# Kernel tuning notes

Measured on AMD Instinct MI355X. Metric: run time of the kernel, lower is better.

Reference implementation:

```python
import jax, jax.numpy as jnp
import numpy as np

B, NQ, NK = 8, 1024, 1024
DQ = DK = DV = 512
H = 8
DH = DV // H
EPS = 1e-5
NEG = -1e9


def _layer_norm(x, g, b):
    mu = jnp.mean(x, axis=-1, keepdims=True)
    var = jnp.mean(jnp.square(x - mu), axis=-1, keepdims=True)
    return (x - mu) * jax.lax.rsqrt(var + EPS) * g + b


def setup_inputs() -> dict:
    key = jax.random.key(0)
    ks = jax.random.split(key, 16)
    s_q = 1.0 / np.sqrt(DQ)
    s_k = 1.0 / np.sqrt(DK)
    s_v = 1.0 / np.sqrt(DV)
    return {
        "Q": jax.random.normal(ks[0], (B, NQ, DQ), jnp.float32),
        "K": jax.random.normal(ks[1], (B, NK, DK), jnp.float32),
        "mask": jax.random.randint(ks[2], (B, NK), 0, 2, jnp.int32),
        "Wq": jax.random.uniform(ks[3], (DQ, DV), jnp.float32, -s_q, s_q),
        "bq": jax.random.uniform(ks[4], (DV,), jnp.float32, -s_q, s_q),
        "Wk": jax.random.uniform(ks[5], (DK, DV), jnp.float32, -s_k, s_k),
        "bk": jax.random.uniform(ks[6], (DV,), jnp.float32, -s_k, s_k),
        "Wv": jax.random.uniform(ks[7], (DK, DV), jnp.float32, -s_k, s_k),
        "bv": jax.random.uniform(ks[8], (DV,), jnp.float32, -s_k, s_k),
        "Wo": jax.random.uniform(ks[9], (DV, DV), jnp.float32, -s_v, s_v),
        "bo": jax.random.uniform(ks[10], (DV,), jnp.float32, -s_v, s_v),
        "g0": jnp.ones((DV,), jnp.float32),
        "b0": jnp.zeros((DV,), jnp.float32),
        "g1": jnp.ones((DV,), jnp.float32),
        "b1": jnp.zeros((DV,), jnp.float32),
    }


def reference(Q, K, mask, Wq, bq, Wk, bk, Wv, bv, Wo, bo, g0, b0, g1, b1):
    b = Q.shape[0]
    # projections: [B, N, DV] -> [B, N, H, DH]
    q = (Q @ Wq + bq).reshape(b, -1, H, DH)
    k = (K @ Wk + bk).reshape(b, -1, H, DH)
    v = (K @ Wv + bv).reshape(b, -1, H, DH)
    scores = jnp.einsum("bqhd,bkhd->bhqk", q, k) / np.sqrt(DH)  # [B,H,Nq,Nk]
    scores = jnp.where((mask == 0)[:, None, None, :], NEG, scores)
    A = jax.nn.softmax(scores, axis=-1)
    o = q + jnp.einsum("bhqk,bkhd->bqhd", A, v)  # residual on projected Q (per head)
    O = o.reshape(b, -1, DV)
    O = _layer_norm(O, g0, b0)
    O = O + jax.nn.relu(O @ Wo + bo)
    O = _layer_norm(O, g1, b1)
    return O
```

## Files before the change

kernel.cpp:

```cpp
#include <hip/hip_runtime.h>


typedef float f32x4 __attribute__((ext_vector_type(4)));
typedef short bf16x8 __attribute__((ext_vector_type(8)));
typedef unsigned short u16;

#define MFMA16 __builtin_amdgcn_mfma_f32_16x16x32_bf16

__device__ __forceinline__ float bf2f(u16 u){
    unsigned x = ((unsigned)u) << 16;
    return __builtin_bit_cast(float, x);
}
__device__ __forceinline__ u16 f2bf(float f){
    unsigned u = __builtin_bit_cast(unsigned, f);
    u = u + 0x7fffu + ((u >> 16) & 1u);
    return (u16)(u >> 16);
}

__global__ __launch_bounds__(256) void transpose_w(
    const float* __restrict__ Wq, const float* __restrict__ Wk,
    const float* __restrict__ Wv, const float* __restrict__ Wo,
    u16* __restrict__ wt)
{
    const int z = blockIdx.z;
    const float* W = (z == 0) ? Wq : (z == 1) ? Wk : (z == 2) ? Wv : Wo;
    u16* out = wt + (size_t)z * 512 * 512;

    __shared__ u16 tile[32][33];
    const int k0 = blockIdx.y * 32, n0 = blockIdx.x * 32;
    const int c = threadIdx.x & 31, r = threadIdx.x >> 5;
#pragma unroll
    for (int i = 0; i < 4; i++) {
        int rr = r + i * 8;
        tile[rr][c] = f2bf(W[(size_t)(k0 + rr) * 512 + n0 + c]);
    }
    __syncthreads();
#pragma unroll
    for (int i = 0; i < 4; i++) {
        int rr = r + i * 8;
        out[(size_t)(n0 + rr) * 512 + k0 + c] = tile[c][rr];
    }
}

__global__ __launch_bounds__(256) void transpose_v(
    const u16* __restrict__ vb, u16* __restrict__ vtg)
{
    __shared__ u16 tile[32][33];
    const int bh = blockIdx.z;
    const int b = bh >> 3, h = bh & 7;
    const int k0 = blockIdx.x * 32, d0 = blockIdx.y * 32;
    const int c = threadIdx.x & 31, r = threadIdx.x >> 5;
#pragma unroll
    for (int i = 0; i < 4; i++) {
        int rr = r + i * 8;
        tile[rr][c] = vb[(size_t)(b * 1024 + k0 + rr) * 512 + h * 64 + d0 + c];
    }
    __syncthreads();
#pragma unroll
    for (int i = 0; i < 4; i++) {
        int rr = r + i * 8;
        vtg[(size_t)(bh * 64 + d0 + rr) * 1024 + k0 + c] = tile[c][rr];
    }
}

__global__ __launch_bounds__(256) void gemm_proj(
    const float* __restrict__ Q, const float* __restrict__ K,
    const u16* __restrict__ wt,
    const float* __restrict__ bq, const float* __restrict__ bk, const float* __restrict__ bv,
    u16* __restrict__ qb, u16* __restrict__ kb, u16* __restrict__ vb)
{
    __shared__ __align__(16) u16 lds_a[128 * 40];
    __shared__ __align__(16) u16 lds_b[128 * 40];

    const int z = blockIdx.z;
    const float* X = (z == 0) ? Q : K;
    const u16* Wt = wt + (size_t)z * 512 * 512;
    const float* bias = (z == 0) ? bq : (z == 1) ? bk : bv;
    u16* outb = (z == 0) ? qb : (z == 1) ? kb : vb;

    const int bm = blockIdx.y, bn = blockIdx.x;
    const int t = threadIdx.x;
    const int wave = t >> 6, lane = t & 63, quad = lane >> 4, lm = lane & 15;
    const int wm = wave >> 1, wn = wave & 1;

    f32x4 acc[4][4];
    const f32x4 zz = {0.f, 0.f, 0.f, 0.f};
#pragma unroll
    for (int i = 0; i < 4; i++)
#pragma unroll
        for (int j = 0; j < 4; j++) acc[i][j] = zz;

    for (int k0 = 0; k0 < 512; k0 += 32) {
#pragma unroll
        for (int i = 0; i < 2; i++) {
            int idx = t + i * 256;
            int r = idx >> 2, c = (idx & 3) * 8;
            const float* xp = &X[(size_t)(bm * 128 + r) * 512 + k0 + c];
            f32x4 a0 = *(const f32x4*)xp;
            f32x4 a1 = *(const f32x4*)(xp + 4);
            bf16x8 xv;
#pragma unroll
            for (int j = 0; j < 4; j++) { xv[j] = (short)f2bf(a0[j]); xv[4 + j] = (short)f2bf(a1[j]); }
            *(bf16x8*)&lds_a[r * 40 + c] = xv;
            *(bf16x8*)&lds_b[r * 40 + c] =
                *(const bf16x8*)&Wt[(size_t)(bn * 128 + r) * 512 + k0 + c];
        }
        __syncthreads();
        bf16x8 af[4], bfr[4];
#pragma unroll
        for (int mi = 0; mi < 4; mi++)
            af[mi] = *(const bf16x8*)&lds_a[(wm * 64 + mi * 16 + lm) * 40 + quad * 8];
#pragma unroll
        for (int ni = 0; ni < 4; ni++)
            bfr[ni] = *(const bf16x8*)&lds_b[(wn * 64 + ni * 16 + lm) * 40 + quad * 8];
#pragma unroll
        for (int mi = 0; mi < 4; mi++)
#pragma unroll
            for (int ni = 0; ni < 4; ni++)
                acc[mi][ni] = MFMA16(af[mi], bfr[ni], acc[mi][ni], 0, 0, 0);
        __syncthreads();
    }

#pragma unroll
    for (int mi = 0; mi < 4; mi++) {
#pragma unroll
        for (int ni = 0; ni < 4; ni++) {
            const int col = bn * 128 + wn * 64 + ni * 16 + lm;
            const float bv_ = bias[col];
#pragma unroll
            for (int r = 0; r < 4; r++) {
                const int row = bm * 128 + wm * 64 + mi * 16 + quad * 4 + r;
                outb[(size_t)row * 512 + col] = f2bf(acc[mi][ni][r] + bv_);
            }
        }
    }
}

__global__ __launch_bounds__(256) void gemm_mlp(
    const u16* __restrict__ X, const u16* __restrict__ wt,
    const float* __restrict__ bo, const float* __restrict__ resid,
    float* __restrict__ outf)
{
    __shared__ __align__(16) u16 lds_a[128 * 40];
    __shared__ __align__(16) u16 lds_b[128 * 40];

    const u16* Wt = wt + (size_t)3 * 512 * 512;
    const int bm = blockIdx.y, bn = blockIdx.x;
    const int t = threadIdx.x;
    const int wave = t >> 6, lane = t & 63, quad = lane >> 4, lm = lane & 15;
    const int wm = wave >> 1, wn = wave & 1;

    f32x4 acc[4][4];
    const f32x4 zz = {0.f, 0.f, 0.f, 0.f};
#pragma unroll
    for (int i = 0; i < 4; i++)
#pragma unroll
        for (int j = 0; j < 4; j++) acc[i][j] = zz;

    for (int k0 = 0; k0 < 512; k0 += 32) {
#pragma unroll
        for (int i = 0; i < 2; i++) {
            int idx = t + i * 256;
            int r = idx >> 2, c = (idx & 3) * 8;
            *(bf16x8*)&lds_a[r * 40 + c] =
                *(const bf16x8*)&X[(size_t)(bm * 128 + r) * 512 + k0 + c];
            *(bf16x8*)&lds_b[r * 40 + c] =
                *(const bf16x8*)&Wt[(size_t)(bn * 128 + r) * 512 + k0 + c];
        }
        __syncthreads();
        bf16x8 af[4], bfr[4];
#pragma unroll
        for (int mi = 0; mi < 4; mi++)
            af[mi] = *(const bf16x8*)&lds_a[(wm * 64 + mi * 16 + lm) * 40 + quad * 8];
#pragma unroll
        for (int ni = 0; ni < 4; ni++)
            bfr[ni] = *(const bf16x8*)&lds_b[(wn * 64 + ni * 16 + lm) * 40 + quad * 8];
#pragma unroll
        for (int mi = 0; mi < 4; mi++)
#pragma unroll
            for (int ni = 0; ni < 4; ni++)
                acc[mi][ni] = MFMA16(af[mi], bfr[ni], acc[mi][ni], 0, 0, 0);
        __syncthreads();
    }

#pragma unroll
    for (int mi = 0; mi < 4; mi++) {
#pragma unroll
        for (int ni = 0; ni < 4; ni++) {
            const int col = bn * 128 + wn * 64 + ni * 16 + lm;
            const float bv_ = bo[col];
#pragma unroll
            for (int r = 0; r < 4; r++) {
                const int row = bm * 128 + wm * 64 + mi * 16 + quad * 4 + r;
                const size_t off = (size_t)row * 512 + col;
                outf[off] = resid[off] + fmaxf(acc[mi][ni][r] + bv_, 0.f);
            }
        }
    }
}

__global__ __launch_bounds__(256) void attn_kernel(
    const u16* __restrict__ qb, const u16* __restrict__ kb, const u16* __restrict__ vtg,
    const int* __restrict__ mask, float* __restrict__ O)
{
    __shared__ __align__(16) u16 k_tile[64 * 88];
    __shared__ __align__(16) u16 vt[64 * 88];
    __shared__ __align__(16) u16 p_st[4 * 32 * 88];
    __shared__ float mskf[1024];

    const int i = blockIdx.x;
    const int s_ = i >> 3;
    const int bh = (i & 7) + 8 * (s_ >> 3);
    const int qt = s_ & 7;
    const int b = bh >> 3, h = bh & 7;

    const int t = threadIdx.x, wave = t >> 6, lane = t & 63;
    const int quad = lane >> 4, lm = lane & 15;
    const int qbase = qt * 128 + wave * 32;
    const size_t baseb = (size_t)b * 1024 * 512;
    const size_t vbase = (size_t)((b * 8 + h) * 64) * 1024;

#pragma unroll
    for (int ii = 0; ii < 4; ii++) {
        int j = t + ii * 256;
        mskf[j] = mask[b * 1024 + j] ? 1.0f : 0.0f;
    }

    bf16x8 aq[2][2];
#pragma unroll
    for (int m = 0; m < 2; m++)
#pragma unroll
        for (int ks = 0; ks < 2; ks++)
            aq[m][ks] = *(const bf16x8*)&qb[baseb +
                (size_t)(qbase + m * 16 + lm) * 512 + h * 64 + ks * 32 + quad * 8];

    float lsum[2][4];
    f32x4 oacc[2][4];
    const f32x4 zz = {0.f, 0.f, 0.f, 0.f};
#pragma unroll
    for (int m = 0; m < 2; m++) {
#pragma unroll
        for (int r = 0; r < 4; r++) lsum[m][r] = 0.f;
#pragma unroll
        for (int c = 0; c < 4; c++) oacc[m][c] = zz;
    }

    const float SC2 = 0.125f * 1.44269504088896341f;
    const int srow = t >> 2, scol = (t & 3) * 16;
    u16* pw = &p_st[wave * 32 * 88];

    for (int kt = 0; kt < 16; ++kt) {
        const int keyg = kt * 64;
        {
            const u16* kp = &kb[baseb + (size_t)(keyg + srow) * 512 + h * 64 + scol];
            *(bf16x8*)&k_tile[srow * 88 + scol]     = *(const bf16x8*)kp;
            *(bf16x8*)&k_tile[srow * 88 + scol + 8] = *(const bf16x8*)(kp + 8);
            const u16* vp = &vtg[vbase + (size_t)srow * 1024 + keyg + scol];
            *(bf16x8*)&vt[srow * 88 + scol]     = *(const bf16x8*)vp;
            *(bf16x8*)&vt[srow * 88 + scol + 8] = *(const bf16x8*)(vp + 8);
        }
        __syncthreads();

        bf16x8 bk[4][2];
#pragma unroll
        for (int n = 0; n < 4; n++)
#pragma unroll
            for (int ks = 0; ks < 2; ks++)
                bk[n][ks] = *(const bf16x8*)&k_tile[(n * 16 + lm) * 88 + ks * 32 + quad * 8];

#pragma unroll
        for (int m = 0; m < 2; m++) {
#pragma unroll
            for (int n = 0; n < 4; n++) {
                f32x4 S = zz;
                S = MFMA16(aq[m][0], bk[n][0], S, 0, 0, 0);
                S = MFMA16(aq[m][1], bk[n][1], S, 0, 0, 0);
                const float mf = mskf[keyg + n * 16 + lm];
#pragma unroll
                for (int r = 0; r < 4; r++) {
                    float p = __builtin_amdgcn_exp2f(S[r] * SC2) * mf;
                    lsum[m][r] += p;
                    pw[(m * 16 + quad * 4 + r) * 88 + n * 16 + lm] = f2bf(p);
                }
            }
        }

#pragma unroll
        for (int m = 0; m < 2; m++) {
#pragma unroll
            for (int ks = 0; ks < 2; ks++) {
                bf16x8 ap = *(const bf16x8*)&pw[(m * 16 + lm) * 88 + ks * 32 + quad * 8];
#pragma unroll
                for (int c = 0; c < 4; c++) {
                    bf16x8 bv_ = *(const bf16x8*)&vt[(c * 16 + lm) * 88 + ks * 32 + quad * 8];
                    oacc[m][c] = MFMA16(ap, bv_, oacc[m][c], 0, 0, 0);
                }
            }
        }
        __syncthreads();
    }

#pragma unroll
    for (int m = 0; m < 2; m++)
#pragma unroll
        for (int r = 0; r < 4; r++) {
            float s = lsum[m][r];
            s += __shfl_xor(s, 1); s += __shfl_xor(s, 2);
            s += __shfl_xor(s, 4); s += __shfl_xor(s, 8);
            lsum[m][r] = s;
        }

#pragma unroll
    for (int m = 0; m < 2; m++)
#pragma unroll
        for (int c = 0; c < 4; c++)
#pragma unroll
            for (int r = 0; r < 4; r++) {
                const int row = qbase + m * 16 + quad * 4 + r;
                const int d = h * 64 + c * 16 + lm;
                const size_t off = baseb + (size_t)row * 512 + d;
                O[off] = bf2f(qb[off]) + oacc[m][c][r] / lsum[m][r];
            }
}

__global__ __launch_bounds__(256) void ln_kernel(
    const float* __restrict__ in, const float* __restrict__ g, const float* __restrict__ bsh,
    u16* __restrict__ outb, float* __restrict__ outf)
{
    const int row = blockIdx.x * 4 + (threadIdx.x >> 6);
    const int lane = threadIdx.x & 63;
    const float* x = in + (size_t)row * 512 + lane * 8;
    float v[8];
    *(f32x4*)&v[0] = *(const f32x4*)&x[0];
    *(f32x4*)&v[4] = *(const f32x4*)&x[4];
    float s = 0.f, sq = 0.f;
#pragma unroll
    for (int j = 0; j < 8; j++) { s += v[j]; sq += v[j] * v[j]; }
#pragma unroll
    for (int off = 1; off < 64; off <<= 1) {
        s += __shfl_xor(s, off);
        sq += __shfl_xor(sq, off);
    }
    const float mu = s * (1.f / 512.f);
    const float var = sq * (1.f / 512.f) - mu * mu;
    const float rs = rsqrtf(var + 1e-5f);
    float y[8];
#pragma unroll
    for (int j = 0; j < 8; j++) {
        int col = lane * 8 + j;
        y[j] = (v[j] - mu) * rs * g[col] + bsh[col];
    }
    if (outb != nullptr) {
        bf16x8 ov;
#pragma unroll
        for (int j = 0; j < 8; j++) ov[j] = (short)f2bf(y[j]);
        *(bf16x8*)&outb[(size_t)row * 512 + lane * 8] = ov;
    }
    if (outf != nullptr) {
        float* o = outf + (size_t)row * 512 + lane * 8;
        *(f32x4*)&o[0] = *(const f32x4*)&y[0];
        *(f32x4*)&o[4] = *(const f32x4*)&y[4];
    }
}

extern "C" void kernel_launch(void* const* d_in, const int* in_sizes, int n_in,
                              void* d_out, int out_size, void* d_ws, size_t ws_size,
                              hipStream_t stream) {
    const float* Q  = (const float*)d_in[0];
    const float* K  = (const float*)d_in[1];
    const int* mask = (const int*)d_in[2];
    const float* Wq = (const float*)d_in[3];
    const float* bq = (const float*)d_in[4];
    const float* Wk = (const float*)d_in[5];
    const float* bk = (const float*)d_in[6];
    const float* Wv = (const float*)d_in[7];
    const float* bv = (const float*)d_in[8];
    const float* Wo = (const float*)d_in[9];
    const float* bo = (const float*)d_in[10];
    const float* g0 = (const float*)d_in[11];
    const float* b0 = (const float*)d_in[12];
    const float* g1 = (const float*)d_in[13];
    const float* b1 = (const float*)d_in[14];
    float* out = (float*)d_out;

    char* ws = (char*)d_ws;
    const size_t MB = 1048576;
    u16*   wt  = (u16*)(ws);
    u16*   qb  = (u16*)(ws + 2 * MB);
    u16*   kb  = (u16*)(ws + 10 * MB);
    u16*   vtg = (u16*)(ws + 18 * MB);
    u16*   vb  = (u16*)(ws + 26 * MB);
    float* Of  = (float*)(ws + 26 * MB);
    u16*   O1b = (u16*)(ws + 2 * MB);
    float* O1f = (float*)(ws + 10 * MB);
    float* Uf  = (float*)(ws + 26 * MB);

    transpose_w<<<dim3(16, 16, 4), 256, 0, stream>>>(Wq, Wk, Wv, Wo, wt);
    gemm_proj<<<dim3(4, 64, 3), 256, 0, stream>>>(Q, K, wt, bq, bk, bv, qb, kb, vb);
    transpose_v<<<dim3(32, 2, 64), 256, 0, stream>>>(vb, vtg);
    attn_kernel<<<512, 256, 0, stream>>>(qb, kb, vtg, mask, Of);
    ln_kernel<<<2048, 256, 0, stream>>>(Of, g0, b0, O1b, O1f);
    gemm_mlp<<<dim3(4, 64, 1), 256, 0, stream>>>(O1b, wt, bo, O1f, Uf);
    ln_kernel<<<2048, 256, 0, stream>>>(Uf, g1, b1, nullptr, out);
}
```

Baseline: 207.1 us.

## Halve attention query tile, prefetch K/V tiles via registers, use additive mask bias

The attention kernel now gives each wave 16 query rows instead of 32 and doubles the grid to 1024 blocks, with launch bounds set to four blocks per CU. The next K/V tile is loaded into registers while the current one is computed, which hides global load latency behind compute. The multiplicative 0/1 mask becomes an additive -30000 bias folded into the exp2 FMA, and s_setprio raises wave priority around the MFMAs. In exchange, each K/V tile is reloaded by twice as many blocks, and the loop keeps four barriers per iteration pair.

```diff
diff --git a/kernel.cpp b/kernel.cpp
--- a/kernel.cpp
+++ b/kernel.cpp
@@ -199,68 +199,71 @@
     }
 }
 
-__global__ __launch_bounds__(256) void attn_kernel(
+__global__ __launch_bounds__(256, 4) void attn_kernel(
     const u16* __restrict__ qb, const u16* __restrict__ kb, const u16* __restrict__ vtg,
     const int* __restrict__ mask, float* __restrict__ O)
 {
     __shared__ __align__(16) u16 k_tile[64 * 88];
     __shared__ __align__(16) u16 vt[64 * 88];
-    __shared__ __align__(16) u16 p_st[4 * 32 * 88];
-    __shared__ float mskf[1024];
+    __shared__ __align__(16) u16 p_st[4 * 16 * 88];
+    __shared__ float mbias[1024];
 
     const int i = blockIdx.x;
     const int s_ = i >> 3;
-    const int bh = (i & 7) + 8 * (s_ >> 3);
-    const int qt = s_ & 7;
+    const int bh = (i & 7) + 8 * (s_ >> 4);
+    const int qt = s_ & 15;
     const int b = bh >> 3, h = bh & 7;
 
     const int t = threadIdx.x, wave = t >> 6, lane = t & 63;
     const int quad = lane >> 4, lm = lane & 15;
-    const int qbase = qt * 128 + wave * 32;
+    const int qbase = qt * 64 + wave * 16;
     const size_t baseb = (size_t)b * 1024 * 512;
     const size_t vbase = (size_t)((b * 8 + h) * 64) * 1024;
 
 #pragma unroll
     for (int ii = 0; ii < 4; ii++) {
         int j = t + ii * 256;
-        mskf[j] = mask[b * 1024 + j] ? 1.0f : 0.0f;
-    }
-
-    bf16x8 aq[2][2];
-#pragma unroll
-    for (int m = 0; m < 2; m++)
-#pragma unroll
-        for (int ks = 0; ks < 2; ks++)
-            aq[m][ks] = *(const bf16x8*)&qb[baseb +
-                (size_t)(qbase + m * 16 + lm) * 512 + h * 64 + ks * 32 + quad * 8];
-
-    float lsum[2][4];
-    f32x4 oacc[2][4];
+        mbias[j] = mask[b * 1024 + j] ? 0.0f : -30000.0f;
+    }
+
+    bf16x8 aq[2];
+#pragma unroll
+    for (int ks = 0; ks < 2; ks++)
+        aq[ks] = *(const bf16x8*)&qb[baseb +
+            (size_t)(qbase + lm) * 512 + h * 64 + ks * 32 + quad * 8];
+
+    float lsum[4] = {0.f, 0.f, 0.f, 0.f};
+    f32x4 oacc[4];
     const f32x4 zz = {0.f, 0.f, 0.f, 0.f};
 #pragma unroll
-    for (int m = 0; m < 2; m++) {
-#pragma unroll
-        for (int r = 0; r < 4; r++) lsum[m][r] = 0.f;
-#pragma unroll
-        for (int c = 0; c < 4; c++) oacc[m][c] = zz;
-    }
+    for (int c = 0; c < 4; c++) oacc[c] = zz;
 
     const float SC2 = 0.125f * 1.44269504088896341f;
     const int srow = t >> 2, scol = (t & 3) * 16;
-    u16* pw = &p_st[wave * 32 * 88];
-
-    for (int kt = 0; kt < 16; ++kt) {
+    u16* pw = &p_st[wave * 16 * 88];
+
+    const u16* kgp = &kb[baseb + (size_t)srow * 512 + h * 64 + scol];
+    const u16* vgp = &vtg[vbase + (size_t)srow * 1024 + scol];
+
+    bf16x8 kA0, kA1, vA0, vA1, kB0, kB1, vB0, vB1;
+
+    auto load_t = [&](int kt, bf16x8& k0, bf16x8& k1, bf16x8& v0, bf16x8& v1) {
+        const u16* kp = kgp + (size_t)kt * 64 * 512;
+        k0 = *(const bf16x8*)kp;
+        k1 = *(const bf16x8*)(kp + 8);
+        const u16* vp = vgp + kt * 64;
+        v0 = *(const bf16x8*)vp;
+        v1 = *(const bf16x8*)(vp + 8);
+    };
+    auto store_t = [&](bf16x8 k0, bf16x8 k1, bf16x8 v0, bf16x8 v1) {
+        *(bf16x8*)&k_tile[srow * 88 + scol]     = k0;
+        *(bf16x8*)&k_tile[srow * 88 + scol + 8] = k1;
+        *(bf16x8*)&vt[srow * 88 + scol]     = v0;
+        *(bf16x8*)&vt[srow * 88 + scol + 8] = v1;
+    };
+
+    auto compute_t = [&](int kt) {
         const int keyg = kt * 64;
-        {
-            const u16* kp = &kb[baseb + (size_t)(keyg + srow) * 512 + h * 64 + scol];
-            *(bf16x8*)&k_tile[srow * 88 + scol]     = *(const bf16x8*)kp;
-            *(bf16x8*)&k_tile[srow * 88 + scol + 8] = *(const bf16x8*)(kp + 8);
-            const u16* vp = &vtg[vbase + (size_t)srow * 1024 + keyg + scol];
-            *(bf16x8*)&vt[srow * 88 + scol]     = *(const bf16x8*)vp;
-            *(bf16x8*)&vt[srow * 88 + scol + 8] = *(const bf16x8*)(vp + 8);
-        }
-        __syncthreads();
-
         bf16x8 bk[4][2];
 #pragma unroll
         for (int n = 0; n < 4; n++)
@@ -269,58 +272,66 @@
                 bk[n][ks] = *(const bf16x8*)&k_tile[(n * 16 + lm) * 88 + ks * 32 + quad * 8];
 
 #pragma unroll
-        for (int m = 0; m < 2; m++) {
-#pragma unroll
-            for (int n = 0; n < 4; n++) {
-                f32x4 S = zz;
-                S = MFMA16(aq[m][0], bk[n][0], S, 0, 0, 0);
-                S = MFMA16(aq[m][1], bk[n][1], S, 0, 0, 0);
-                const float mf = mskf[keyg + n * 16 + lm];
-#pragma unroll
-                for (int r = 0; r < 4; r++) {
-                    float p = __builtin_amdgcn_exp2f(S[r] * SC2) * mf;
-                    lsum[m][r] += p;
-                    pw[(m * 16 + quad * 4 + r) * 88 + n * 16 + lm] = f2bf(p);
-                }
+        for (int n = 0; n < 4; n++) {
+            f32x4 S = zz;
+            __builtin_amdgcn_s_setprio(1);
+            S = MFMA16(aq[0], bk[n][0], S, 0, 0, 0);
+            S = MFMA16(aq[1], bk[n][1], S, 0, 0, 0);
+            __builtin_amdgcn_s_setprio(0);
+            const float bias = mbias[keyg + n * 16 + lm];
+#pragma unroll
+            for (int r = 0; r < 4; r++) {
+                float p = __builtin_amdgcn_exp2f(__builtin_fmaf(S[r], SC2, bias));
+                lsum[r] += p;
+                pw[(quad * 4 + r) * 88 + n * 16 + lm] = f2bf(p);
             }
         }
 
 #pragma unroll
-        for (int m = 0; m < 2; m++) {
-#pragma unroll
-            for (int ks = 0; ks < 2; ks++) {
-                bf16x8 ap = *(const bf16x8*)&pw[(m * 16 + lm) * 88 + ks * 32 + quad * 8];
-#pragma unroll
-                for (int c = 0; c < 4; c++) {
-                    bf16x8 bv_ = *(const bf16x8*)&vt[(c * 16 + lm) * 88 + ks * 32 + quad * 8];
-                    oacc[m][c] = MFMA16(ap, bv_, oacc[m][c], 0, 0, 0);
-                }
+        for (int ks = 0; ks < 2; ks++) {
+            bf16x8 ap = *(const bf16x8*)&pw[lm * 88 + ks * 32 + quad * 8];
+            __builtin_amdgcn_s_setprio(1);
+#pragma unroll
+            for (int c = 0; c < 4; c++) {
+                bf16x8 bv_ = *(const bf16x8*)&vt[(c * 16 + lm) * 88 + ks * 32 + quad * 8];
+                oacc[c] = MFMA16(ap, bv_, oacc[c], 0, 0, 0);
             }
-        }
-        __syncthreads();
-    }
-
-#pragma unroll
-    for (int m = 0; m < 2; m++)
+            __builtin_amdgcn_s_setprio(0);
+        }
+    };
+
+    load_t(0, kA0, kA1, vA0, vA1);
+
+    for (int kt = 0; kt < 16; kt += 2) {
+        store_t(kA0, kA1, vA0, vA1);
+        load_t(kt + 1, kB0, kB1, vB0, vB1);
+        __syncthreads();
+        compute_t(kt);
+        __syncthreads();
+        store_t(kB0, kB1, vB0, vB1);
+        load_t((kt + 2) & 15, kA0, kA1, vA0, vA1);
+        __syncthreads();
+        compute_t(kt + 1);
+        __syncthreads();
+    }
+
+#pragma unroll
+    for (int r = 0; r < 4; r++) {
+        float s = lsum[r];
+        s += __shfl_xor(s, 1); s += __shfl_xor(s, 2);
+        s += __shfl_xor(s, 4); s += __shfl_xor(s, 8);
+        lsum[r] = s;
+    }
+
+#pragma unroll
+    for (int c = 0; c < 4; c++)
 #pragma unroll
         for (int r = 0; r < 4; r++) {
-            float s = lsum[m][r];
-            s += __shfl_xor(s, 1); s += __shfl_xor(s, 2);
-            s += __shfl_xor(s, 4); s += __shfl_xor(s, 8);
-            lsum[m][r] = s;
-        }
-
-#pragma unroll
-    for (int m = 0; m < 2; m++)
-#pragma unroll
-        for (int c = 0; c < 4; c++)
-#pragma unroll
-            for (int r = 0; r < 4; r++) {
-                const int row = qbase + m * 16 + quad * 4 + r;
-                const int d = h * 64 + c * 16 + lm;
-                const size_t off = baseb + (size_t)row * 512 + d;
-                O[off] = bf2f(qb[off]) + oacc[m][c][r] / lsum[m][r];
-            }
+            const int row = qbase + quad * 4 + r;
+            const int d = h * 64 + c * 16 + lm;
+            const size_t off = baseb + (size_t)row * 512 + d;
+            O[off] = bf2f(qb[off]) + oacc[c][r] / lsum[r];
+        }
 }
 
 __global__ __launch_bounds__(256) void ln_kernel(
@@ -398,7 +409,7 @@
     transpose_w<<<dim3(16, 16, 4), 256, 0, stream>>>(Wq, Wk, Wv, Wo, wt);
     gemm_proj<<<dim3(4, 64, 3), 256, 0, stream>>>(Q, K, wt, bq, bk, bv, qb, kb, vb);
     transpose_v<<<dim3(32, 2, 64), 256, 0, stream>>>(vb, vtg);
-    attn_kernel<<<512, 256, 0, stream>>>(qb, kb, vtg, mask, Of);
+    attn_kernel<<<1024, 256, 0, stream>>>(qb, kb, vtg, mask, Of);
     ln_kernel<<<2048, 256, 0, stream>>>(Of, g0, b0, O1b, O1f);
     gemm_mlp<<<dim3(4, 64, 1), 256, 0, stream>>>(O1b, wt, bo, O1f, Uf);
     ln_kernel<<<2048, 256, 0, stream>>>(Uf, g1, b1, nullptr, out);
```

Result: no change. 207.4 us (+0.2%).

## Load K/V fragments directly from global, drop LDS staging and block syncs

Applied to the files above, without the earlier changes.

The attention kernel drops its shared-memory K and V tiles and the per-tile __syncthreads. Each wave now loads its MFMA K and V fragments straight from global memory into registers. Blocks shrink to 2 waves over 64 queries, so the grid doubles to 1024 blocks. The mask becomes an additive -30000 bias fused into the exp2 argument, and MFMA sections are wrapped in s_setprio. The aim is to remove LDS round-trips and barrier stalls, at the cost of redundant global/L2 traffic, since each wave now refetches the same K/V rows.

```diff
diff --git a/kernel.cpp b/kernel.cpp
--- a/kernel.cpp
+++ b/kernel.cpp
@@ -199,32 +199,24 @@
     }
 }
 
-__global__ __launch_bounds__(256) void attn_kernel(
+__global__ __launch_bounds__(128, 3) void attn_kernel(
     const u16* __restrict__ qb, const u16* __restrict__ kb, const u16* __restrict__ vtg,
     const int* __restrict__ mask, float* __restrict__ O)
 {
-    __shared__ __align__(16) u16 k_tile[64 * 88];
-    __shared__ __align__(16) u16 vt[64 * 88];
-    __shared__ __align__(16) u16 p_st[4 * 32 * 88];
-    __shared__ float mskf[1024];
+    __shared__ __align__(16) u16 p_st[2 * 32 * 88];
 
     const int i = blockIdx.x;
     const int s_ = i >> 3;
-    const int bh = (i & 7) + 8 * (s_ >> 3);
-    const int qt = s_ & 7;
+    const int bh = (i & 7) + 8 * (s_ >> 4);
+    const int qt = s_ & 15;
     const int b = bh >> 3, h = bh & 7;
 
     const int t = threadIdx.x, wave = t >> 6, lane = t & 63;
     const int quad = lane >> 4, lm = lane & 15;
-    const int qbase = qt * 128 + wave * 32;
+    const int qbase = qt * 64 + wave * 32;
     const size_t baseb = (size_t)b * 1024 * 512;
     const size_t vbase = (size_t)((b * 8 + h) * 64) * 1024;
-
-#pragma unroll
-    for (int ii = 0; ii < 4; ii++) {
-        int j = t + ii * 256;
-        mskf[j] = mask[b * 1024 + j] ? 1.0f : 0.0f;
-    }
+    const int* mrow = &mask[b * 1024];
 
     bf16x8 aq[2][2];
 #pragma unroll
@@ -246,39 +238,44 @@
     }
 
     const float SC2 = 0.125f * 1.44269504088896341f;
-    const int srow = t >> 2, scol = (t & 3) * 16;
     u16* pw = &p_st[wave * 32 * 88];
 
     for (int kt = 0; kt < 16; ++kt) {
         const int keyg = kt * 64;
-        {
-            const u16* kp = &kb[baseb + (size_t)(keyg + srow) * 512 + h * 64 + scol];
-            *(bf16x8*)&k_tile[srow * 88 + scol]     = *(const bf16x8*)kp;
-            *(bf16x8*)&k_tile[srow * 88 + scol + 8] = *(const bf16x8*)(kp + 8);
-            const u16* vp = &vtg[vbase + (size_t)srow * 1024 + keyg + scol];
-            *(bf16x8*)&vt[srow * 88 + scol]     = *(const bf16x8*)vp;
-            *(bf16x8*)&vt[srow * 88 + scol + 8] = *(const bf16x8*)(vp + 8);
-        }
-        __syncthreads();
-
-        bf16x8 bk[4][2];
+
+        bf16x8 bkf[4][2];
 #pragma unroll
         for (int n = 0; n < 4; n++)
 #pragma unroll
             for (int ks = 0; ks < 2; ks++)
-                bk[n][ks] = *(const bf16x8*)&k_tile[(n * 16 + lm) * 88 + ks * 32 + quad * 8];
+                bkf[n][ks] = *(const bf16x8*)&kb[baseb +
+                    (size_t)(keyg + n * 16 + lm) * 512 + h * 64 + ks * 32 + quad * 8];
+
+        bf16x8 bvf[4][2];
+#pragma unroll
+        for (int c = 0; c < 4; c++)
+#pragma unroll
+            for (int ks = 0; ks < 2; ks++)
+                bvf[c][ks] = *(const bf16x8*)&vtg[vbase +
+                    (size_t)(c * 16 + lm) * 1024 + keyg + ks * 32 + quad * 8];
+
+        float bias[4];
+#pragma unroll
+        for (int n = 0; n < 4; n++)
+            bias[n] = mrow[keyg + n * 16 + lm] ? 0.0f : -30000.0f;
 
 #pragma unroll
         for (int m = 0; m < 2; m++) {
 #pragma unroll
             for (int n = 0; n < 4; n++) {
                 f32x4 S = zz;
-                S = MFMA16(aq[m][0], bk[n][0], S, 0, 0, 0);
-                S = MFMA16(aq[m][1], bk[n][1], S, 0, 0, 0);
-                const float mf = mskf[keyg + n * 16 + lm];
+                __builtin_amdgcn_s_setprio(1);
+                S = MFMA16(aq[m][0], bkf[n][0], S, 0, 0, 0);
+                S = MFMA16(aq[m][1], bkf[n][1], S, 0, 0, 0);
+                __builtin_amdgcn_s_setprio(0);
 #pragma unroll
                 for (int r = 0; r < 4; r++) {
-                    float p = __builtin_amdgcn_exp2f(S[r] * SC2) * mf;
+                    float p = __builtin_amdgcn_exp2f(__builtin_fmaf(S[r], SC2, bias[n]));
                     lsum[m][r] += p;
                     pw[(m * 16 + quad * 4 + r) * 88 + n * 16 + lm] = f2bf(p);
                 }
@@ -290,14 +287,13 @@
 #pragma unroll
             for (int ks = 0; ks < 2; ks++) {
                 bf16x8 ap = *(const bf16x8*)&pw[(m * 16 + lm) * 88 + ks * 32 + quad * 8];
-#pragma unroll
-                for (int c = 0; c < 4; c++) {
-                    bf16x8 bv_ = *(const bf16x8*)&vt[(c * 16 + lm) * 88 + ks * 32 + quad * 8];
-                    oacc[m][c] = MFMA16(ap, bv_, oacc[m][c], 0, 0, 0);
-                }
+                __builtin_amdgcn_s_setprio(1);
+#pragma unroll
+                for (int c = 0; c < 4; c++)
+                    oacc[m][c] = MFMA16(ap, bvf[c][ks], oacc[m][c], 0, 0, 0);
+                __builtin_amdgcn_s_setprio(0);
             }
         }
-        __syncthreads();
     }
 
 #pragma unroll
@@ -398,7 +394,7 @@
     transpose_w<<<dim3(16, 16, 4), 256, 0, stream>>>(Wq, Wk, Wv, Wo, wt);
     gemm_proj<<<dim3(4, 64, 3), 256, 0, stream>>>(Q, K, wt, bq, bk, bv, qb, kb, vb);
     transpose_v<<<dim3(32, 2, 64), 256, 0, stream>>>(vb, vtg);
-    attn_kernel<<<512, 256, 0, stream>>>(qb, kb, vtg, mask, Of);
+    attn_kernel<<<1024, 128, 0, stream>>>(qb, kb, vtg, mask, Of);
     ln_kernel<<<2048, 256, 0, stream>>>(Of, g0, b0, O1b, O1f);
     gemm_mlp<<<dim3(4, 64, 1), 256, 0, stream>>>(O1b, wt, bo, O1f, Uf);
     ln_kernel<<<2048, 256, 0, stream>>>(Uf, g1, b1, nullptr, out);
```

After: 237.5 us. 1.15x slower.
